# Kernel optimization log

Hardware: AMD Instinct MI355X
Metric: run time of the kernel (lower is better)

The kernel has to match this reference:

```python
import jax, jax.numpy as jnp
import numpy as np

D = 2            # stalk dimension d
FD = 3           # final_d = d + 1 (add_lp=True, add_hp=False)
HID = 32         # hidden_channels
N_NODES = 50000
E0 = 200000      # undirected edges; directed edge list has 2*E0 entries (second half reversed)
IN_CH = 128
OUT_CH = 32
N_LAYERS = 2
PSIZE = D * (D + 1) // 2  # cayley param size per edge


def _spectral_normalize(W, iters=20):
    # torch spectral_norm: power iteration with detached u, v; sigma = u^T W v
    u = jnp.full((W.shape[0],), 1.0 / np.sqrt(W.shape[0]), W.dtype)
    def body(_, u):
        v = W.T @ u
        v = v / (jnp.linalg.norm(v) + 1e-12)
        u2 = W @ v
        return u2 / (jnp.linalg.norm(u2) + 1e-12)
    u = jax.lax.fori_loop(0, iters, body, u)
    u = jax.lax.stop_gradient(u)
    v = jax.lax.stop_gradient(W.T @ u)
    v = v / (jnp.linalg.norm(v) + 1e-12)
    return W / (u @ W @ v)


def _cayley(p):
    # p: [E, PSIZE] lower-tri params -> skew A -> orthogonal Q = (I - A)^{-1}(I + A)
    E = p.shape[0]
    r, c = jnp.tril_indices(D)
    M = jnp.zeros((E, D, D), p.dtype).at[:, r, c].set(p)
    A = M - jnp.swapaxes(M, 1, 2)
    I = jnp.eye(D, dtype=p.dtype)
    return jnp.linalg.solve(I[None] - A, I[None] + A)


def setup_inputs() -> dict:
    key = jax.random.key(0)
    ks = jax.random.split(key, 8)
    src = jax.random.randint(ks[0], (E0,), 0, N_NODES)
    dst = jax.random.randint(ks[1], (E0,), 0, N_NODES)
    # symmetric directed edge list; edge j and edge j+E0 are reverses of each other
    edge_index = jnp.concatenate([jnp.stack([src, dst]), jnp.stack([dst, src])], axis=1)
    x = jax.random.normal(ks[2], (N_NODES, IN_CH), jnp.float32)
    s = 0.02
    W1 = jax.random.normal(ks[3], (FD * HID, IN_CH), jnp.float32) * s
    b1 = jnp.zeros((FD * HID,), jnp.float32)
    W2 = jax.random.normal(ks[4], (OUT_CH, FD * HID), jnp.float32) * s
    b2 = jnp.zeros((OUT_CH,), jnp.float32)
    W_left = jnp.tile(jnp.eye(FD, dtype=jnp.float32)[None], (N_LAYERS, 1, 1))  # init eye per torch
    W_right = jax.random.normal(ks[5], (N_LAYERS, HID, HID), jnp.float32) / np.sqrt(HID)
    eps = jnp.zeros((N_LAYERS, FD, 1), jnp.float32)
    W_sheaf = jax.random.normal(ks[6], (N_LAYERS, PSIZE, 2 * FD * HID), jnp.float32) * s
    W_wt = jax.random.normal(ks[7], (N_LAYERS, 1, 2 * FD * HID), jnp.float32) * s
    return {"x": x, "edge_index": edge_index, "W1": W1, "b1": b1, "W2": W2, "b2": b2,
            "W_left": W_left, "W_right": W_right, "eps": eps, "W_sheaf": W_sheaf, "W_wt": W_wt}


def reference(x, edge_index, W1, b1, W2, b2, W_left, W_right, eps, W_sheaf, W_wt):
    N = x.shape[0]
    row, col = edge_index[0], edge_index[1]
    e0 = row.shape[0] // 2
    rev = jnp.concatenate([jnp.arange(e0) + e0, jnp.arange(e0)])  # reverse-edge index
    # lin1 + ELU (dropouts = 0 in eval)
    h = jax.nn.elu(x @ W1.T + b1)                 # [N, FD*HID]
    xc = h.reshape(N * FD, HID)                   # [N*FD, HID]
    x0 = xc
    for layer in range(N_LAYERS):
        # --- sheaf learner + edge weight learner (gather endpoint features) ---
        xn = xc.reshape(N, FD * HID)
        cat = jnp.concatenate([xn[row], xn[col]], axis=-1)   # [2*E0, 2*FD*HID]
        p = jnp.tanh(cat @ W_sheaf[layer].T)                 # sheaf map params [2*E0, PSIZE]
        wdir = jax.nn.sigmoid(cat @ W_wt[layer].T)[:, 0]
        w = wdir * wdir[rev]                                 # symmetric edge weight
        # --- normalized connection (bundle) Laplacian ---
        Q = _cayley(p)                                       # per-edge orthogonal maps
        T = jnp.einsum('eij,eik->ejk', Q, Q[rev])            # transport F_u^T F_v
        w2 = w * w
        deg = jax.ops.segment_sum(w2, row, num_segments=N)
        dinv = jnp.where(deg > 0, jax.lax.rsqrt(jnp.maximum(deg, 1e-30)), 0.0)
        cnorm = w2 * dinv[row] * dinv[col]                   # [2*E0]
        # --- left / right weights (spectral-normalized) ---
        Wl = _spectral_normalize(W_left[layer])
        Wr = _spectral_normalize(W_right[layer])
        y = xc.reshape(N, FD, HID)
        y = jnp.einsum('ef,nfh->neh', Wl, y)                 # mix stalk dims
        y = jnp.einsum('neh,ch->nec', y, Wr)                 # mix channels
        # --- apply block-sparse Laplacian: Lx[u] = x[u] - sum_e c_e B_e x[v] ---
        yv = y[col]                                          # gather  [2*E0, FD, HID]
        tv = jnp.concatenate([jnp.einsum('eij,ejh->eih', T, yv[:, :D]), yv[:, D:]], axis=1)
        agg = jax.ops.segment_sum(cnorm[:, None, None] * tv, row, num_segments=N)
        diag = jnp.where(deg > 0, 1.0, 0.0)[:, None, None]
        z = jax.nn.elu((diag * y - agg).reshape(N * FD, HID))
        # --- epsilon-gated residual ---
        coeff = jnp.tile(1.0 + jnp.tanh(eps[layer]), (N, 1))  # [N*FD, 1]
        x0 = coeff * x0 - z
        xc = x0
    return xc.reshape(N, FD * HID) @ W2.T + b2
```

## Files before the change

kernel.cpp:

```cpp
#include <hip/hip_runtime.h>

#define NN 50000
#define E0 200000
#define E2 400000
#define NGROUPS ((NN + 7) / 8)
#define NG4     ((NN + 3) / 4)
#define NCHUNK  ((NN + 255) / 256)
#define NTILES  ((NN + 63) / 64)
#define EB      ((E2 + 255) / 256)

typedef __attribute__((ext_vector_type(8))) short short8;
typedef __attribute__((ext_vector_type(4))) float f32x4;

__device__ __forceinline__ float eluf(float x) { return x > 0.0f ? x : expm1f(x); }
__device__ __forceinline__ float fsig(float x) { return 1.0f / (1.0f + __expf(-x)); }
__device__ __forceinline__ float ftanh(float x) {
    float e = __expf(-2.0f * x);
    return (1.0f - e) / (1.0f + e);
}
__device__ __forceinline__ unsigned rne_bf16(float x) {
    unsigned u = __float_as_uint(x);
    return (u + 0x7fffu + ((u >> 16) & 1u)) >> 16;
}

__global__ __launch_bounds__(256) void k_setup(int* __restrict__ cnt, int* __restrict__ fill,
                                               float* __restrict__ deg0, int* __restrict__ gtotal) {
    int i = blockIdx.x * 256 + threadIdx.x;
    if (i == 0) *gtotal = 0;
    if (i < NN) { cnt[i] = 0; fill[i] = 0; deg0[i] = 0.0f; }
}

__device__ __forceinline__ void spectral_block(int l, const float* __restrict__ Wl_in,
                                               const float* __restrict__ Wr_in,
                                               float* __restrict__ Wl_out, float* __restrict__ Wr_out) {
    __shared__ float W[32 * 33];
    __shared__ float us[32], vs[32], tmp[32];
    __shared__ float scal;
    int t = threadIdx.x;
    for (int i = t; i < 1024; i += 256) W[(i >> 5) * 33 + (i & 31)] = Wr_in[l * 1024 + i];
    if (t < 32) us[t] = 0.17677669529663688f;
    __syncthreads();
    for (int it = 0; it < 20; ++it) {
        if (t < 32) { float a = 0; for (int r = 0; r < 32; ++r) a = fmaf(W[r * 33 + t], us[r], a); tmp[t] = a; }
        __syncthreads();
        if (t == 0) { float s = 0; for (int c = 0; c < 32; ++c) s += tmp[c] * tmp[c]; scal = 1.0f / (sqrtf(s) + 1e-12f); }
        __syncthreads();
        if (t < 32) vs[t] = tmp[t] * scal;
        __syncthreads();
        if (t < 32) { float a = 0; for (int c = 0; c < 32; ++c) a = fmaf(W[t * 33 + c], vs[c], a); tmp[t] = a; }
        __syncthreads();
        if (t == 0) { float s = 0; for (int r = 0; r < 32; ++r) s += tmp[r] * tmp[r]; scal = 1.0f / (sqrtf(s) + 1e-12f); }
        __syncthreads();
        if (t < 32) us[t] = tmp[t] * scal;
        __syncthreads();
    }
    if (t < 32) { float a = 0; for (int r = 0; r < 32; ++r) a = fmaf(W[r * 33 + t], us[r], a); tmp[t] = a; }
    __syncthreads();
    if (t == 0) {
        float s = 0; for (int c = 0; c < 32; ++c) s += tmp[c] * tmp[c];
        scal = (sqrtf(s) + 1e-12f) / s;
    }
    __syncthreads();
    for (int i = t; i < 1024; i += 256) Wr_out[l * 1024 + i] = W[(i >> 5) * 33 + (i & 31)] * scal;
    if (t == 0) {
        float M[9];
        for (int i = 0; i < 9; ++i) M[i] = Wl_in[l * 9 + i];
        float u[3] = {0.5773502691896258f, 0.5773502691896258f, 0.5773502691896258f};
        float v[3], u2[3];
        for (int it = 0; it < 20; ++it) {
            float s = 0;
            for (int c = 0; c < 3; ++c) { v[c] = M[c] * u[0] + M[3 + c] * u[1] + M[6 + c] * u[2]; s += v[c] * v[c]; }
            float inv = 1.0f / (sqrtf(s) + 1e-12f);
            for (int c = 0; c < 3; ++c) v[c] *= inv;
            s = 0;
            for (int r = 0; r < 3; ++r) { u2[r] = M[r * 3] * v[0] + M[r * 3 + 1] * v[1] + M[r * 3 + 2] * v[2]; s += u2[r] * u2[r]; }
            inv = 1.0f / (sqrtf(s) + 1e-12f);
            for (int r = 0; r < 3; ++r) u[r] = u2[r] * inv;
        }
        float s = 0;
        for (int c = 0; c < 3; ++c) { v[c] = M[c] * u[0] + M[3 + c] * u[1] + M[6 + c] * u[2]; s += v[c] * v[c]; }
        float inv = (sqrtf(s) + 1e-12f) / s;
        for (int i = 0; i < 9; ++i) Wl_out[l * 9 + i] = M[i] * inv;
    }
}

template<int K, int N, int NH, bool ELU, bool AUX>
__global__ __launch_bounds__(256) void k_gemm(const float* __restrict__ X,
                                              const float* __restrict__ W,
                                              const float* __restrict__ bias,
                                              float* __restrict__ out,
                                              const int* __restrict__ row, int* __restrict__ cnt,
                                              const float* __restrict__ Wl_in, const float* __restrict__ Wr_in,
                                              float* __restrict__ Wl_out, float* __restrict__ Wr_out) {
    constexpr int KP = K + 8;
    constexpr int NT = NH / 16;
    constexpr int KS = K / 32;
    constexpr int NHALVES = N / NH;
    const int nmain = AUX ? (int)gridDim.x - 2 : (int)gridDim.x;
    if constexpr (AUX) {
        if ((int)blockIdx.x >= nmain) {
            spectral_block((int)blockIdx.x - nmain, Wl_in, Wr_in, Wl_out, Wr_out);
            return;
        }
    }
    __shared__ __align__(16) unsigned short whi[NH * KP];
    __shared__ __align__(16) unsigned short wlo[NH * KP];
    int tid = threadIdx.x;
    if constexpr (AUX) {
        for (int e = blockIdx.x * 256 + tid; e < E2; e += nmain * 256)
            atomicAdd(&cnt[row[e]], 1);
    }
    const int ch = blockIdx.x % NHALVES;
    const int tstream = blockIdx.x / NHALVES;
    const int nstreams = nmain / NHALVES;
    for (int i = tid; i < NH * K; i += 256) {
        float v = W[ch * NH * K + i];
        int r = i / K, c = i % K;
        unsigned h = rne_bf16(v);
        whi[r * KP + c] = (unsigned short)h;
        wlo[r * KP + c] = (unsigned short)rne_bf16(v - __uint_as_float(h << 16));
    }
    __syncthreads();
    int wave = tid >> 6, lane = tid & 63;
    int quad = lane >> 4, r16 = lane & 15;
    for (int t = tstream; t < NTILES; t += nstreams) {
        long m = (long)t * 64 + wave * 16 + r16;
        long mc = m < NN ? m : (NN - 1);
        const float* xrow = X + mc * K + quad * 8;
        short8 ah[KS], al[KS];
#pragma unroll
        for (int ks = 0; ks < KS; ++ks) {
            const float4* xp = (const float4*)(xrow + ks * 32);
            float4 p0 = xp[0], p1 = xp[1];
            float xv[8] = {p0.x, p0.y, p0.z, p0.w, p1.x, p1.y, p1.z, p1.w};
#pragma unroll
            for (int j = 0; j < 8; ++j) {
                unsigned h = rne_bf16(xv[j]);
                ah[ks][j] = (short)h;
                al[ks][j] = (short)rne_bf16(xv[j] - __uint_as_float(h << 16));
            }
        }
        long mbase = (long)t * 64 + wave * 16 + quad * 4;
#pragma unroll
        for (int tt = 0; tt < NT; ++tt) {
            f32x4 acc = (f32x4){0.f, 0.f, 0.f, 0.f};
#pragma unroll
            for (int ks = 0; ks < KS; ++ks) {
                int ro = (tt * 16 + r16) * KP + ks * 32 + quad * 8;
                short8 bh = *(const short8*)&whi[ro];
                short8 bl = *(const short8*)&wlo[ro];
                acc = __builtin_amdgcn_mfma_f32_16x16x32_bf16(ah[ks], bh, acc, 0, 0, 0);
                acc = __builtin_amdgcn_mfma_f32_16x16x32_bf16(al[ks], bh, acc, 0, 0, 0);
                acc = __builtin_amdgcn_mfma_f32_16x16x32_bf16(ah[ks], bl, acc, 0, 0, 0);
            }
            int coln = ch * NH + tt * 16 + r16;
            float b = bias[coln];
#pragma unroll
            for (int rr = 0; rr < 4; ++rr) {
                long mm = mbase + rr;
                if (mm < NN) {
                    float v = acc[rr] + b;
                    if (ELU) v = eluf(v);
                    out[mm * N + coln] = v;
                }
            }
        }
    }
}

__global__ __launch_bounds__(256) void k_scan(const int* __restrict__ cnt, int* __restrict__ start,
                                              int* __restrict__ gtotal) {
    __shared__ int s[256];
    __shared__ int soff;
    int b = blockIdx.x, t = threadIdx.x;
    int i = b * 256 + t;
    int v = (i < NN) ? cnt[i] : 0;
    s[t] = v;
    __syncthreads();
    for (int off = 1; off < 256; off <<= 1) {
        int add = (t >= off) ? s[t - off] : 0;
        __syncthreads();
        s[t] += add;
        __syncthreads();
    }
    if (t == 255) soff = atomicAdd(gtotal, s[255]);
    __syncthreads();
    if (i < NN) start[i] = s[t] - v + soff;
}

__global__ __launch_bounds__(256) void k_filly8(const float* __restrict__ xc,
                                                const float* __restrict__ Wl, const float* __restrict__ Wr,
                                                const float* __restrict__ Wsh, const float* __restrict__ Wwt,
                                                uint2* __restrict__ yAB,
                                                float4* __restrict__ proj,
                                                const int* __restrict__ row, const int* __restrict__ start,
                                                int* __restrict__ fill, int* __restrict__ eslot) {
    int tid = threadIdx.x;
    if (blockIdx.x >= NGROUPS) {
        int e = (blockIdx.x - NGROUPS) * 256 + tid;
        if (e < E2) {
            int u = row[e];
            eslot[e] = start[u] + atomicAdd(&fill[u], 1);
        }
        return;
    }
    __shared__ float wrs[32 * 33];
    __shared__ float wls[9];
    __shared__ float xcs[8][96];
    __shared__ float ws1[192], wt[192];
    int n0 = blockIdx.x * 8;
    for (int i = tid; i < 1024; i += 256) wrs[(i >> 5) * 33 + (i & 31)] = Wr[i];
    if (tid < 9) wls[tid] = Wl[tid];
    if (tid < 192) {
        ws1[tid] = Wsh[192 + tid];
        wt[tid]  = Wwt[tid];
    }
    for (int i = tid; i < 192; i += 256) {
        int nd = i / 24, of = (i % 24) * 4;
        *(float4*)&xcs[nd][of] = *(const float4*)&xc[(n0 + nd) * 96 + of];
    }
    __syncthreads();
    int node = tid >> 5, c = tid & 31;
    int n = n0 + node;
    float a1 = 0, a2 = 0, a3 = 0, a4 = 0;
#pragma unroll
    for (int j = 0; j < 3; ++j) {
        int k = j * 32 + c;
        float xv = xcs[node][k];
        a1 = fmaf(xv, ws1[k], a1);
        a2 = fmaf(xv, ws1[96 + k], a2);
        a3 = fmaf(xv, wt[k], a3);
        a4 = fmaf(xv, wt[96 + k], a4);
    }
#pragma unroll
    for (int off = 16; off; off >>= 1) {
        a1 += __shfl_xor(a1, off);
        a2 += __shfl_xor(a2, off);
        a3 += __shfl_xor(a3, off);
        a4 += __shfl_xor(a4, off);
    }
    if (c == 0) proj[n] = make_float4(a1, a2, a3, a4);
    {
        float t0 = 0, t1 = 0, t2 = 0;
        const float* wr = &wrs[c * 33];
        const float* xr = xcs[node];
#pragma unroll
        for (int h = 0; h < 32; ++h) {
            float w = wr[h];
            t0 = fmaf(xr[h], w, t0);
            t1 = fmaf(xr[32 + h], w, t1);
            t2 = fmaf(xr[64 + h], w, t2);
        }
        float o0 = wls[0] * t0 + wls[1] * t1 + wls[2] * t2;
        float o1 = wls[3] * t0 + wls[4] * t1 + wls[5] * t2;
        float o2 = wls[6] * t0 + wls[7] * t1 + wls[8] * t2;
        yAB[n * 32 + c] = make_uint2(rne_bf16(o0) | (rne_bf16(o1) << 16), rne_bf16(o2) << 16);
    }
}

__global__ __launch_bounds__(256) void k_coef(const int* __restrict__ row, const int* __restrict__ col,
                                              const int* __restrict__ eslot,
                                              const float4* __restrict__ proj,
                                              uint2* __restrict__ meta, float* __restrict__ deg) {
    int e = blockIdx.x * 256 + threadIdx.x;
    if (e >= E0) return;
    int u = row[e], v = col[e];
    float4 pu = proj[u], pv = proj[v];
    float a_e = ftanh(pu.x + pv.y);
    float a_r = ftanh(pv.x + pu.y);
    float wd_e = fsig(pu.z + pv.w);
    float wd_r = fsig(pv.z + pu.w);
    float w = wd_e * wd_r;
    float w2 = w * w;
    float ie = 1.0f / (1.0f + a_e * a_e), ir = 1.0f / (1.0f + a_r * a_r);
    float ce = (1.0f - a_e * a_e) * ie, se = 2.0f * a_e * ie;
    float cr = (1.0f - a_r * a_r) * ir, sr = 2.0f * a_r * ir;
    float C = ce * cr + se * sr;
    float S = ce * sr - se * cr;
    unsigned cb = rne_bf16(C), sb = rne_bf16(S), wb = rne_bf16(w2);
    meta[eslot[e]]      = make_uint2(cb | (sb << 16), (unsigned)v | (wb << 16));
    meta[eslot[e + E0]] = make_uint2(cb | ((sb ^ 0x8000u) << 16), (unsigned)u | (wb << 16));
    atomicAdd(&deg[u], w2);
    atomicAdd(&deg[v], w2);
}

__device__ __forceinline__ void gather_accum(int s0, int ec, int h, int c,
                                             const uint2* __restrict__ meta,
                                             const float* __restrict__ deg, float du,
                                             const uint2* __restrict__ yAB,
                                             float& acc0, float& acc1, float& acc2) {
    const uint2* yc = yAB + c;
    for (int bs = 0; bs < ec; bs += 64) {
        int nb = min(64, ec - bs);
        float CC = 0, SS = 0, cnl = 0;
        int vj = 0;
        int eidx = 2 * c + h;
        if (eidx < nb) {
            uint2 mt = meta[s0 + bs + eidx];
            vj = (int)(mt.y & 0xffffu);
            float w2 = __uint_as_float(mt.y & 0xffff0000u);
            float Cv = __uint_as_float(mt.x << 16);
            float Sv = __uint_as_float(mt.x & 0xffff0000u);
            float dv = deg[vj];
            float dvi = dv > 0.0f ? rsqrtf(fmaxf(dv, 1e-30f)) : 0.0f;
            cnl = w2 * du * dvi;
            CC = cnl * Cv;
            SS = cnl * Sv;
        }
        int jmax = (nb + 1 - h) >> 1;
        int j4 = jmax & ~3;
        int j = 0;
        for (; j < j4; j += 4) {
#pragma unroll
            for (int jj = 0; jj < 4; ++jj) {
                float Cj = __shfl(CC, j + jj, 32);
                float Sj = __shfl(SS, j + jj, 32);
                float cj = __shfl(cnl, j + jj, 32);
                int v = __shfl(vj, j + jj, 32);
                uint2 y = yc[v * 32];
                float y0 = __uint_as_float(y.x << 16);
                float y1 = __uint_as_float(y.x & 0xffff0000u);
                float y2 = __uint_as_float(y.y);
                acc0 = fmaf(Cj, y0, acc0);
                acc0 = fmaf(-Sj, y1, acc0);
                acc1 = fmaf(Sj, y0, acc1);
                acc1 = fmaf(Cj, y1, acc1);
                acc2 = fmaf(cj, y2, acc2);
            }
        }
        for (; j < jmax; ++j) {
            float Cj = __shfl(CC, j, 32);
            float Sj = __shfl(SS, j, 32);
            float cj = __shfl(cnl, j, 32);
            int v = __shfl(vj, j, 32);
            uint2 y = yc[v * 32];
            float y0 = __uint_as_float(y.x << 16);
            float y1 = __uint_as_float(y.x & 0xffff0000u);
            float y2 = __uint_as_float(y.y);
            acc0 = fmaf(Cj, y0, acc0);
            acc0 = fmaf(-Sj, y1, acc0);
            acc1 = fmaf(Sj, y0, acc1);
            acc1 = fmaf(Cj, y1, acc1);
            acc2 = fmaf(cj, y2, acc2);
        }
    }
}

__global__ __launch_bounds__(256) void k_gatherY(const int* __restrict__ start,
                                                 const int* __restrict__ cnt,
                                                 const uint2* __restrict__ meta,
                                                 const float* __restrict__ deg0,
                                                 const uint2* __restrict__ yAB0,
                                                 const float* __restrict__ eps,
                                                 float* __restrict__ xc,
                                                 const float* __restrict__ Wl, const float* __restrict__ Wr,
                                                 const float* __restrict__ Wsh, const float* __restrict__ Wwt,
                                                 uint2* __restrict__ yAB1,
                                                 float4* __restrict__ proj, float* __restrict__ deg1) {
    __shared__ float wrs[32 * 33];
    __shared__ float wls[9];
    __shared__ float xcs[4][96];
    __shared__ float ws1[192], wt[192];
    int tid = threadIdx.x;
    for (int i = tid; i < 1024; i += 256) wrs[(i >> 5) * 33 + (i & 31)] = Wr[i];
    if (tid < 9) wls[tid] = Wl[tid];
    if (tid < 192) {
        ws1[tid] = Wsh[(1 * 3 + 1) * 192 + tid];
        wt[tid]  = Wwt[192 + tid];
    }
    int wv = tid >> 6, lane = tid & 63, h = lane >> 5, c = lane & 31;
    int n = blockIdx.x * 4 + wv;
    int s0 = start[n], ec = cnt[n];
    float dn = deg0[n];
    float du = dn > 0.0f ? rsqrtf(fmaxf(dn, 1e-30f)) : 0.0f;
    int base = n * 96 + c;
    float xv0 = xc[base], xv1 = xc[base + 32], xv2 = xc[base + 64];
    uint2 yown = yAB0[n * 32 + c];
    float c0 = 1.0f + tanhf(eps[0]);
    float c1 = 1.0f + tanhf(eps[1]);
    float c2 = 1.0f + tanhf(eps[2]);
    __syncthreads();
    float acc0 = 0, acc1 = 0, acc2 = 0;
    gather_accum(s0, ec, h, c, meta, deg0, du, yAB0, acc0, acc1, acc2);
    acc0 += __shfl_xor(acc0, 32);
    acc1 += __shfl_xor(acc1, 32);
    acc2 += __shfl_xor(acc2, 32);
    float diag = dn > 0.0f ? 1.0f : 0.0f;
    float oy0 = __uint_as_float(yown.x << 16);
    float oy1 = __uint_as_float(yown.x & 0xffff0000u);
    float oy2 = __uint_as_float(yown.y);
    float nx0 = c0 * xv0 - eluf(diag * oy0 - acc0);
    float nx1 = c1 * xv1 - eluf(diag * oy1 - acc1);
    float nx2 = c2 * xv2 - eluf(diag * oy2 - acc2);
    if (h == 0) {
        xc[base] = nx0; xc[base + 32] = nx1; xc[base + 64] = nx2;
        xcs[wv][c] = nx0; xcs[wv][32 + c] = nx1; xcs[wv][64 + c] = nx2;
        if (c == 0) deg1[n] = 0.0f;
    }
    float a1 = nx0 * ws1[c] + nx1 * ws1[32 + c] + nx2 * ws1[64 + c];
    float a2 = nx0 * ws1[96 + c] + nx1 * ws1[128 + c] + nx2 * ws1[160 + c];
    float a3 = nx0 * wt[c] + nx1 * wt[32 + c] + nx2 * wt[64 + c];
    float a4 = nx0 * wt[96 + c] + nx1 * wt[128 + c] + nx2 * wt[160 + c];
#pragma unroll
    for (int off = 16; off; off >>= 1) {
        a1 += __shfl_xor(a1, off);
        a2 += __shfl_xor(a2, off);
        a3 += __shfl_xor(a3, off);
        a4 += __shfl_xor(a4, off);
    }
    if (lane == 0) proj[n] = make_float4(a1, a2, a3, a4);
    __syncthreads();
    float t0 = 0, t1 = 0, t2 = 0;
    const float* wr = &wrs[c * 33 + h * 16];
    const float* xr = &xcs[wv][h * 16];
#pragma unroll
    for (int k = 0; k < 16; ++k) {
        float w = wr[k];
        t0 = fmaf(xr[k], w, t0);
        t1 = fmaf(xr[32 + k], w, t1);
        t2 = fmaf(xr[64 + k], w, t2);
    }
    t0 += __shfl_xor(t0, 32);
    t1 += __shfl_xor(t1, 32);
    t2 += __shfl_xor(t2, 32);
    if (h == 0) {
        float o0 = wls[0] * t0 + wls[1] * t1 + wls[2] * t2;
        float o1 = wls[3] * t0 + wls[4] * t1 + wls[5] * t2;
        float o2 = wls[6] * t0 + wls[7] * t1 + wls[8] * t2;
        yAB1[n * 32 + c] = make_uint2(rne_bf16(o0) | (rne_bf16(o1) << 16), rne_bf16(o2) << 16);
    }
}

__global__ __launch_bounds__(256) void k_gather(const int* __restrict__ start,
                                                const int* __restrict__ cnt,
                                                const uint2* __restrict__ meta,
                                                const float* __restrict__ deg,
                                                const uint2* __restrict__ yAB,
                                                const float* __restrict__ eps,
                                                int layer, float* __restrict__ xc) {
    int tid = threadIdx.x;
    int lane = tid & 63, h = lane >> 5, c = lane & 31;
    int n = blockIdx.x * 4 + (tid >> 6);
    int s0 = start[n], ec = cnt[n];
    float dn = deg[n];
    float du = dn > 0.0f ? rsqrtf(fmaxf(dn, 1e-30f)) : 0.0f;
    int base = n * 96 + c;
    float xv0 = xc[base], xv1 = xc[base + 32], xv2 = xc[base + 64];
    uint2 yown = yAB[n * 32 + c];
    float c0 = 1.0f + tanhf(eps[layer * 3 + 0]);
    float c1 = 1.0f + tanhf(eps[layer * 3 + 1]);
    float c2 = 1.0f + tanhf(eps[layer * 3 + 2]);
    float acc0 = 0, acc1 = 0, acc2 = 0;
    gather_accum(s0, ec, h, c, meta, deg, du, yAB, acc0, acc1, acc2);
    acc0 += __shfl_xor(acc0, 32);
    acc1 += __shfl_xor(acc1, 32);
    acc2 += __shfl_xor(acc2, 32);
    if (h == 0) {
        float diag = dn > 0.0f ? 1.0f : 0.0f;
        float oy0 = __uint_as_float(yown.x << 16);
        float oy1 = __uint_as_float(yown.x & 0xffff0000u);
        float oy2 = __uint_as_float(yown.y);
        xc[base]      = c0 * xv0 - eluf(diag * oy0 - acc0);
        xc[base + 32] = c1 * xv1 - eluf(diag * oy1 - acc1);
        xc[base + 64] = c2 * xv2 - eluf(diag * oy2 - acc2);
    }
}

extern "C" void kernel_launch(void* const* d_in, const int* in_sizes, int n_in,
                              void* d_out, int out_size, void* d_ws, size_t ws_size,
                              hipStream_t stream) {
    const float* x     = (const float*)d_in[0];
    const int*   ei    = (const int*)d_in[1];
    const float* W1    = (const float*)d_in[2];
    const float* b1    = (const float*)d_in[3];
    const float* W2    = (const float*)d_in[4];
    const float* b2    = (const float*)d_in[5];
    const float* Wl    = (const float*)d_in[6];
    const float* Wr    = (const float*)d_in[7];
    const float* eps   = (const float*)d_in[8];
    const float* Wsh   = (const float*)d_in[9];
    const float* Wwt   = (const float*)d_in[10];
    float* out = (float*)d_out;
    const int* row = ei;
    const int* col = ei + E2;

    char* pc = (char*)d_ws;
    float* xc     = (float*)pc;          pc += (size_t)NN * 96 * 4;
    uint2* meta   = (uint2*)pc;          pc += (size_t)E2 * 8;
    uint2* yAB0   = (uint2*)pc;          pc += (size_t)NN * 32 * 8;
    uint2* yAB1   = (uint2*)pc;          pc += (size_t)NN * 32 * 8;
    pc = (char*)(((size_t)pc + 15) & ~(size_t)15);
    float4* proj  = (float4*)pc;         pc += (size_t)NN * 16;
    float* deg0   = (float*)pc;          pc += (size_t)NN * 4;
    float* deg1   = (float*)pc;          pc += (size_t)NN * 4;
    float* Wl_n   = (float*)pc;          pc += 32 * 4;
    float* Wr_n   = (float*)pc;          pc += 2048 * 4;
    int* cnt      = (int*)pc;            pc += (size_t)NN * 4;
    int* start    = (int*)pc;            pc += (size_t)NN * 4;
    int* fill     = (int*)pc;            pc += (size_t)NN * 4;
    int* eslot    = (int*)pc;            pc += (size_t)E2 * 4;
    int* gtotal   = (int*)pc;            pc += 4;

    k_setup<<<NCHUNK, 256, 0, stream>>>(cnt, fill, deg0, gtotal);
    k_gemm<128, 96, 48, true, true><<<514, 256, 0, stream>>>(x, W1, b1, xc, row, cnt,
                                                             Wl, Wr, Wl_n, Wr_n);
    k_scan<<<NCHUNK, 256, 0, stream>>>(cnt, start, gtotal);
    k_filly8<<<NGROUPS + EB, 256, 0, stream>>>(xc, Wl_n, Wr_n, Wsh, Wwt,
                                               yAB0, proj, row, start, fill, eslot);
    k_coef<<<(E0 + 255) / 256, 256, 0, stream>>>(row, col, eslot, proj, meta, deg0);
    k_gatherY<<<NG4, 256, 0, stream>>>(start, cnt, meta, deg0, yAB0, eps, xc,
                                       Wl_n + 9, Wr_n + 1024, Wsh, Wwt, yAB1, proj, deg1);
    k_coef<<<(E0 + 255) / 256, 256, 0, stream>>>(row, col, eslot, proj, meta, deg1);
    k_gather<<<NG4, 256, 0, stream>>>(start, cnt, meta, deg1, yAB1, eps, 1, xc);
    k_gemm<96, 32, 32, false, false><<<512, 256, 0, stream>>>(xc, W2, b2, out, nullptr, nullptr,
                                                              nullptr, nullptr, nullptr, nullptr);
}
```

Measured before the change: 327.9 us.

## Move spectral normalization into setup kernel with shuffle-based power iteration

The spectral-normalization power iteration moves out of the first GEMM's auxiliary blocks and into the setup kernel. It is rewritten to use wave shuffles and reductions instead of shared-memory round trips and many block barriers, and the 3x3 left-weight iteration now runs on a separate wave in parallel. This keeps two slow serial blocks from extending the GEMM's tail. The GEMM grid sizes are also raised (514→1024, 512→782), which spreads tiles more finely but reloads weights into shared memory in more blocks.

Result: no change. 328.2 us (+0.1%).

```diff
diff --git a/kernel.cpp b/kernel.cpp
--- a/kernel.cpp
+++ b/kernel.cpp
@@ -23,46 +23,40 @@
     return (u + 0x7fffu + ((u >> 16) & 1u)) >> 16;
 }
 
-__global__ __launch_bounds__(256) void k_setup(int* __restrict__ cnt, int* __restrict__ fill,
-                                               float* __restrict__ deg0, int* __restrict__ gtotal) {
-    int i = blockIdx.x * 256 + threadIdx.x;
-    if (i == 0) *gtotal = 0;
-    if (i < NN) { cnt[i] = 0; fill[i] = 0; deg0[i] = 0.0f; }
-}
-
 __device__ __forceinline__ void spectral_block(int l, const float* __restrict__ Wl_in,
                                                const float* __restrict__ Wr_in,
                                                float* __restrict__ Wl_out, float* __restrict__ Wr_out) {
     __shared__ float W[32 * 33];
-    __shared__ float us[32], vs[32], tmp[32];
-    __shared__ float scal;
+    __shared__ float sscal;
     int t = threadIdx.x;
     for (int i = t; i < 1024; i += 256) W[(i >> 5) * 33 + (i & 31)] = Wr_in[l * 1024 + i];
-    if (t < 32) us[t] = 0.17677669529663688f;
-    __syncthreads();
-    for (int it = 0; it < 20; ++it) {
-        if (t < 32) { float a = 0; for (int r = 0; r < 32; ++r) a = fmaf(W[r * 33 + t], us[r], a); tmp[t] = a; }
-        __syncthreads();
-        if (t == 0) { float s = 0; for (int c = 0; c < 32; ++c) s += tmp[c] * tmp[c]; scal = 1.0f / (sqrtf(s) + 1e-12f); }
-        __syncthreads();
-        if (t < 32) vs[t] = tmp[t] * scal;
-        __syncthreads();
-        if (t < 32) { float a = 0; for (int c = 0; c < 32; ++c) a = fmaf(W[t * 33 + c], vs[c], a); tmp[t] = a; }
-        __syncthreads();
-        if (t == 0) { float s = 0; for (int r = 0; r < 32; ++r) s += tmp[r] * tmp[r]; scal = 1.0f / (sqrtf(s) + 1e-12f); }
-        __syncthreads();
-        if (t < 32) us[t] = tmp[t] * scal;
-        __syncthreads();
-    }
-    if (t < 32) { float a = 0; for (int r = 0; r < 32; ++r) a = fmaf(W[r * 33 + t], us[r], a); tmp[t] = a; }
-    __syncthreads();
-    if (t == 0) {
-        float s = 0; for (int c = 0; c < 32; ++c) s += tmp[c] * tmp[c];
-        scal = (sqrtf(s) + 1e-12f) / s;
-    }
-    __syncthreads();
-    for (int i = t; i < 1024; i += 256) Wr_out[l * 1024 + i] = W[(i >> 5) * 33 + (i & 31)] * scal;
-    if (t == 0) {
+    __syncthreads();
+    if (t < 32) {
+        float u = 0.17677669529663688f;
+        for (int it = 0; it < 20; ++it) {
+            float v = 0.f;
+#pragma unroll 8
+            for (int r = 0; r < 32; ++r) v = fmaf(W[r * 33 + t], __shfl(u, r, 32), v);
+            float s = v * v;
+#pragma unroll
+            for (int off = 16; off; off >>= 1) s += __shfl_xor(s, off, 32);
+            v *= 1.0f / (sqrtf(s) + 1e-12f);
+            float u2 = 0.f;
+#pragma unroll 8
+            for (int c = 0; c < 32; ++c) u2 = fmaf(W[t * 33 + c], __shfl(v, c, 32), u2);
+            s = u2 * u2;
+#pragma unroll
+            for (int off = 16; off; off >>= 1) s += __shfl_xor(s, off, 32);
+            u = u2 * (1.0f / (sqrtf(s) + 1e-12f));
+        }
+        float v = 0.f;
+#pragma unroll 8
+        for (int r = 0; r < 32; ++r) v = fmaf(W[r * 33 + t], __shfl(u, r, 32), v);
+        float s = v * v;
+#pragma unroll
+        for (int off = 16; off; off >>= 1) s += __shfl_xor(s, off, 32);
+        if (t == 0) sscal = (sqrtf(s) + 1e-12f) / s;
+    } else if (t == 64) {
         float M[9];
         for (int i = 0; i < 9; ++i) M[i] = Wl_in[l * 9 + i];
         float u[3] = {0.5773502691896258f, 0.5773502691896258f, 0.5773502691896258f};
@@ -82,37 +76,44 @@
         float inv = (sqrtf(s) + 1e-12f) / s;
         for (int i = 0; i < 9; ++i) Wl_out[l * 9 + i] = M[i] * inv;
     }
-}
-
-template<int K, int N, int NH, bool ELU, bool AUX>
+    __syncthreads();
+    float invs = sscal;
+    for (int i = t; i < 1024; i += 256) Wr_out[l * 1024 + i] = W[(i >> 5) * 33 + (i & 31)] * invs;
+}
+
+__global__ __launch_bounds__(256) void k_setup(const float* __restrict__ Wl_in, const float* __restrict__ Wr_in,
+                                               float* __restrict__ Wl_out, float* __restrict__ Wr_out,
+                                               int* __restrict__ cnt, int* __restrict__ fill,
+                                               float* __restrict__ deg0, int* __restrict__ gtotal) {
+    if (blockIdx.x < 2) {
+        spectral_block((int)blockIdx.x, Wl_in, Wr_in, Wl_out, Wr_out);
+        return;
+    }
+    int i = (blockIdx.x - 2) * 256 + threadIdx.x;
+    if (i == 0) *gtotal = 0;
+    if (i < NN) { cnt[i] = 0; fill[i] = 0; deg0[i] = 0.0f; }
+}
+
+template<int K, int N, int NH, bool ELU, bool HIST>
 __global__ __launch_bounds__(256) void k_gemm(const float* __restrict__ X,
                                               const float* __restrict__ W,
                                               const float* __restrict__ bias,
                                               float* __restrict__ out,
-                                              const int* __restrict__ row, int* __restrict__ cnt,
-                                              const float* __restrict__ Wl_in, const float* __restrict__ Wr_in,
-                                              float* __restrict__ Wl_out, float* __restrict__ Wr_out) {
+                                              const int* __restrict__ row, int* __restrict__ cnt) {
     constexpr int KP = K + 8;
     constexpr int NT = NH / 16;
     constexpr int KS = K / 32;
     constexpr int NHALVES = N / NH;
-    const int nmain = AUX ? (int)gridDim.x - 2 : (int)gridDim.x;
-    if constexpr (AUX) {
-        if ((int)blockIdx.x >= nmain) {
-            spectral_block((int)blockIdx.x - nmain, Wl_in, Wr_in, Wl_out, Wr_out);
-            return;
-        }
-    }
     __shared__ __align__(16) unsigned short whi[NH * KP];
     __shared__ __align__(16) unsigned short wlo[NH * KP];
     int tid = threadIdx.x;
-    if constexpr (AUX) {
-        for (int e = blockIdx.x * 256 + tid; e < E2; e += nmain * 256)
+    if (HIST) {
+        for (int e = blockIdx.x * 256 + tid; e < E2; e += gridDim.x * 256)
             atomicAdd(&cnt[row[e]], 1);
     }
     const int ch = blockIdx.x % NHALVES;
     const int tstream = blockIdx.x / NHALVES;
-    const int nstreams = nmain / NHALVES;
+    const int nstreams = gridDim.x / NHALVES;
     for (int i = tid; i < NH * K; i += 256) {
         float v = W[ch * NH * K + i];
         int r = i / K, c = i % K;
@@ -501,9 +502,8 @@
     int* eslot    = (int*)pc;            pc += (size_t)E2 * 4;
     int* gtotal   = (int*)pc;            pc += 4;
 
-    k_setup<<<NCHUNK, 256, 0, stream>>>(cnt, fill, deg0, gtotal);
-    k_gemm<128, 96, 48, true, true><<<514, 256, 0, stream>>>(x, W1, b1, xc, row, cnt,
-                                                             Wl, Wr, Wl_n, Wr_n);
+    k_setup<<<NCHUNK + 2, 256, 0, stream>>>(Wl, Wr, Wl_n, Wr_n, cnt, fill, deg0, gtotal);
+    k_gemm<128, 96, 48, true, true><<<1024, 256, 0, stream>>>(x, W1, b1, xc, row, cnt);
     k_scan<<<NCHUNK, 256, 0, stream>>>(cnt, start, gtotal);
     k_filly8<<<NGROUPS + EB, 256, 0, stream>>>(xc, Wl_n, Wr_n, Wsh, Wwt,
                                                yAB0, proj, row, start, fill, eslot);
@@ -512,6 +512,5 @@
                                        Wl_n + 9, Wr_n + 1024, Wsh, Wwt, yAB1, proj, deg1);
     k_coef<<<(E0 + 255) / 256, 256, 0, stream>>>(row, col, eslot, proj, meta, deg1);
     k_gather<<<NG4, 256, 0, stream>>>(start, cnt, meta, deg1, yAB1, eps, 1, xc);
-    k_gemm<96, 32, 32, false, false><<<512, 256, 0, stream>>>(xc, W2, b2, out, nullptr, nullptr,
-                                                              nullptr, nullptr, nullptr, nullptr);
-}
+    k_gemm<96, 32, 32, false, false><<<782, 256, 0, stream>>>(xc, W2, b2, out, nullptr, nullptr);
+}
```
